# Kernel optimization log

Hardware: AMD Instinct MI355X
Metric: run time of the kernel (lower is better)

The kernel has to match this reference:

```python
import jax, jax.numpy as jnp
import numpy as np

N_ELEC, N_NUC, D, F, E = 1024, 256, 64, 64, 131072
HH, HG = 128, 128
# labels: en (elec->nuc), ne (nuc->elec), same (elec->elec), anti (elec->elec)
SRC_N = [N_ELEC, N_NUC, N_ELEC, N_ELEC]
TGT_N = [N_NUC, N_ELEC, N_ELEC, N_ELEC]


def setup_inputs() -> dict:
    key = jax.random.key(0)
    ks = jax.random.split(key, 16)
    s_elec = jax.random.normal(ks[0], (N_ELEC, D), jnp.float32)
    v_elec = jax.random.normal(ks[1], (N_ELEC, D, 3), jnp.float32)
    s_nuc = jax.random.normal(ks[2], (N_NUC, D), jnp.float32)
    v_nuc = jax.random.normal(ks[3], (N_NUC, D, 3), jnp.float32)
    senders = jnp.stack([jax.random.randint(jax.random.fold_in(ks[4], i), (E,), 0, SRC_N[i]) for i in range(4)]).astype(jnp.int32)
    receivers = jnp.stack([jax.random.randint(jax.random.fold_in(ks[5], i), (E,), 0, TGT_N[i]) for i in range(4)]).astype(jnp.int32)
    dist = jax.random.uniform(ks[6], (4, E, F), jnp.float32)
    dirs = jax.random.normal(ks[7], (4, E, 3), jnp.float32)
    dirs = dirs / jnp.linalg.norm(dirs, axis=-1, keepdims=True)  # unit directions
    def w_init(k, shape):
        return jax.random.normal(k, shape, jnp.float32) / jnp.sqrt(jnp.float32(shape[-2]))
    return {
        's_elec': s_elec, 'v_elec': v_elec, 's_nuc': s_nuc, 'v_nuc': v_nuc,
        'dist': dist, 'dirs': dirs,
        'W_w': w_init(ks[8], (4, F, 3 * D)),
        'W_h1': w_init(ks[9], (4, D, HH)), 'W_h2': w_init(ks[10], (4, HH, 3 * D)),
        'W_g1': w_init(ks[11], (4, 2 * D, HG)), 'W_g2': w_init(ks[12], (4, HG, 3 * D)),
        'W_V': jnp.broadcast_to(jnp.eye(D, dtype=jnp.float32), (4, D, D)),
        'W_U': jnp.broadcast_to(jnp.eye(D, dtype=jnp.float32), (4, D, D)),
        'senders': senders, 'receivers': receivers,
    }


def _painn_layer(s_elec, v_elec, s_nuc, v_nuc, dist, dirs, W_w, W_h1, W_h2, W_g1, W_g2, W_V, W_U, senders, receivers):
    src_s = [s_elec, s_nuc, s_elec, s_elec]
    src_v = [v_elec, v_nuc, v_elec, v_elec]
    ds_e = jnp.zeros_like(s_elec); dv_e = jnp.zeros_like(v_elec)
    ds_n = jnp.zeros_like(s_nuc); dv_n = jnp.zeros_like(v_nuc)
    for i in range(4):
        n_tgt = TGT_N[i]
        # edge MLPs: w (1-layer, last linear) and h (2-layer silu, last linear), bias-free
        we = dist[i] @ W_w[i]                                   # [E, 3D]
        h_all = jax.nn.silu(src_s[i] @ W_h1[i]) @ W_h2[i]        # [n_src, 3D]
        hx = h_all[senders[i]]                                   # gather per edge
        phi_s, phi_vv, phi_vs = jnp.split(we * hx, 3, axis=-1)   # each [E, D]
        z_s = jax.ops.segment_sum(phi_s, receivers[i], n_tgt)    # [n_tgt, D]
        vv = phi_vv[..., None] * src_v[i][senders[i]]            # [E, D, 3]
        vs = phi_vs[..., None] * dirs[i][:, None, :]             # [E, D, 3]
        z_v = jax.ops.segment_sum(vv + vs, receivers[i], n_tgt)  # [n_tgt, D, 3]
        Vv = jnp.einsum('ndi,df->nfi', z_v, W_V[i])
        Uv = jnp.einsum('ndi,df->nfi', z_v, W_U[i])
        g_in = jnp.concatenate([z_s, (Vv ** 2).sum(axis=-1)], axis=-1)  # [n_tgt, 2D]
        gs = jax.nn.silu(g_in @ W_g1[i]) @ W_g2[i]               # [n_tgt, 3D]
        a_ss, a_vv, a_sv = jnp.split(gs, 3, axis=-1)
        upd_v = Uv * a_vv[..., None]
        upd_s = a_sv * jnp.einsum('nfi,nfi->nf', Uv, Vv) + a_ss
        if i == 0:  # 'en' -> nuclei
            ds_n = ds_n + upd_s; dv_n = dv_n + upd_v
        else:       # 'ne','same','anti' -> electrons
            ds_e = ds_e + upd_s; dv_e = dv_e + upd_v
    s_e = s_elec + ds_e
    v_e = v_elec + dv_e
    return jnp.concatenate([s_e, v_e.reshape(N_ELEC, -1)], axis=-1)


def reference(s_elec, v_elec, s_nuc, v_nuc, dist, dirs, W_w, W_h1, W_h2, W_g1, W_g2, W_V, W_U, senders, receivers):
    return _painn_layer(s_elec, v_elec, s_nuc, v_nuc, dist, dirs, W_w, W_h1, W_h2, W_g1, W_g2, W_V, W_U, senders, receivers)
```

## Files before the change

### kernel.cpp

```cpp
#include <hip/hip_runtime.h>
#include <stdint.h>

#define E_EDGES 131072
#define NELEC 1024
#define NNUC 256
#define MAXCHUNK 256
#define NBLK 16

typedef __attribute__((ext_vector_type(8))) short short8;
typedef __attribute__((ext_vector_type(4))) short short4_t;
typedef __attribute__((ext_vector_type(4))) float float4_t;
typedef __attribute__((ext_vector_type(4))) int int4_t;

__device__ inline float silu_f(float x){ return x / (1.0f + expf(-x)); }

__device__ inline short f2bf_rne(float x){
    union { float f; uint32_t u; } a; a.f = x;
    return (short)((a.u + 0x7fffu + ((a.u >> 16) & 1u)) >> 16);
}
__device__ inline float bf2f(short h){
    union { uint32_t u; float f; } a; a.u = ((uint32_t)(uint16_t)h) << 16;
    return a.f;
}

__global__ __launch_bounds__(256) void prep_kernel(
    const float* __restrict__ s_elec, const float* __restrict__ v_elec,
    const float* __restrict__ s_nuc,
    const float* __restrict__ W_h1, const float* __restrict__ W_h2,
    const float* __restrict__ W_w,
    const int* __restrict__ receivers,
    float* __restrict__ h_out, short* __restrict__ fragH, short* __restrict__ fragL,
    int* __restrict__ bh, float* __restrict__ out)
{
    int b = blockIdx.x, tid = threadIdx.x;
    __shared__ float sls[8][64];
    __shared__ float hidls[128][8];
    __shared__ int hist[1024];

    if (b < 288){
        int t, node0;
        if (b < 32){ t = 0; node0 = b*8; }
        else if (b < 160){ t = 1; node0 = (b-32)*8; }
        else { t = 2; node0 = (b-160)*8; }
        int tp = t + 1;
        const float* src = (t == 0) ? s_nuc : s_elec;
        long hbase = (t == 0) ? 0 : (t == 1 ? (long)NNUC*192 : (long)NNUC*192 + (long)NELEC*192);
        for (int i = tid; i < 512; i += 256){ int n = i >> 6, f = i & 63; sls[n][f] = src[(node0+n)*64 + f]; }
        __syncthreads();
        {
            int j = tid & 127, nh = tid >> 7;
            const float* w1 = W_h1 + (long)tp*64*128;
            float a0=0,a1=0,a2=0,a3=0;
            #pragma unroll 8
            for (int f = 0; f < 64; f++){
                float w = w1[f*128 + j];
                a0 += sls[nh*4+0][f]*w; a1 += sls[nh*4+1][f]*w;
                a2 += sls[nh*4+2][f]*w; a3 += sls[nh*4+3][f]*w;
            }
            float4_t hv = { silu_f(a0), silu_f(a1), silu_f(a2), silu_f(a3) };
            *(float4_t*)&hidls[j][nh*4] = hv;
        }
        __syncthreads();
        if (tid < 192){
            const float* w2 = W_h2 + (long)tp*128*192;
            float acc[8] = {0,0,0,0,0,0,0,0};
            #pragma unroll 4
            for (int h = 0; h < 128; h++){
                float w = w2[h*192 + tid];
                float4_t ha = *(float4_t*)&hidls[h][0];
                float4_t hb = *(float4_t*)&hidls[h][4];
                acc[0]+=ha[0]*w; acc[1]+=ha[1]*w; acc[2]+=ha[2]*w; acc[3]+=ha[3]*w;
                acc[4]+=hb[0]*w; acc[5]+=hb[1]*w; acc[6]+=hb[2]*w; acc[7]+=hb[3]*w;
            }
            #pragma unroll
            for (int n = 0; n < 8; n++) h_out[hbase + (long)(node0+n)*192 + tid] = acc[n];
        }
    } else if (b < 291){
        int t = b - 288, tp = t + 1;
        const float* W = W_w + (long)tp*64*192;
        for (int idx = tid; idx < 12288; idx += 256){
            int j    = idx & 7;
            int lane = (idx >> 3) & 63;
            int ks   = (idx >> 9) & 1;
            int nt   = idx >> 10;
            int k = ks*32 + ((lane >> 4) & 3)*8 + j;
            int n = nt*16 + (lane & 15);
            float v = W[k*192 + n];
            short hi = f2bf_rne(v);
            short lo = f2bf_rne(v - bf2f(hi));
            fragH[t*12288 + idx] = hi;
            fragL[t*12288 + idx] = lo;
        }
    } else if (b < 547){
        int i = (b - 291)*256 + tid;
        int n = i >> 6, c4 = i & 63;
        float4_t v;
        if (c4 < 16) v = *(const float4_t*)(s_elec + n*64 + c4*4);
        else         v = *(const float4_t*)(v_elec + n*192 + (c4-16)*4);
        *(float4_t*)(out + n*256 + c4*4) = v;
    } else {
        int hb = b - 547, t = hb >> 4, blk = hb & 15;
        for (int i = tid; i < 1024; i += 256) hist[i] = 0;
        __syncthreads();
        long base = (long)(t+1)*E_EDGES + blk*8192;
        #pragma unroll 4
        for (int it = 0; it < 32; it++){
            int r = receivers[base + it*256 + tid];
            atomicAdd(&hist[r], 1);
        }
        __syncthreads();
        for (int bin = tid; bin < 1024; bin += 256)
            bh[(t*1024 + bin)*NBLK + blk] = hist[bin];
    }
}

__global__ __launch_bounds__(1024) void scan_kernel(int* __restrict__ bh,
                                                    int* __restrict__ offs,
                                                    int* __restrict__ counts){
    __shared__ int buf[1024];
    int tid = threadIdx.x;
    int base = tid*48;
    int vals[48];
    const int4_t* p = (const int4_t*)(bh + base);
    int s = 0;
    #pragma unroll
    for (int j = 0; j < 12; j++){
        int4_t x = p[j];
        vals[j*4+0]=x[0]; vals[j*4+1]=x[1]; vals[j*4+2]=x[2]; vals[j*4+3]=x[3];
        s += x[0]+x[1]+x[2]+x[3];
    }
    buf[tid] = s;
    __syncthreads();
    int x = s;
    for (int off = 1; off < 1024; off <<= 1){
        int y = (tid >= off) ? buf[tid - off] : 0;
        __syncthreads();
        x += y; buf[tid] = x;
        __syncthreads();
    }
    int run = x - s;
    #pragma unroll
    for (int k = 0; k < 3; k++){
        int tb = tid*3 + k;
        offs[tb] = run;
        int c = 0;
        #pragma unroll
        for (int j = 0; j < 16; j++){
            int v = vals[k*16 + j];
            bh[base + k*16 + j] = run;
            run += v; c += v;
        }
        counts[tb] = c;
    }
}

__global__ __launch_bounds__(256) void scatter_kernel(const int* __restrict__ receivers,
                                                      const int* __restrict__ senders,
                                                      const int* __restrict__ bh,
                                                      int* __restrict__ sorted){
    int hb = blockIdx.x, t = hb >> 4, blk = hb & 15;
    int tid = threadIdx.x;
    __shared__ int cur[1024];
    for (int bin = tid; bin < 1024; bin += 256) cur[bin] = bh[(t*1024 + bin)*NBLK + blk];
    __syncthreads();
    long base = (long)(t+1)*E_EDGES + blk*8192;
    #pragma unroll 2
    for (int it = 0; it < 32; it++){
        int e = blk*8192 + it*256 + tid;
        int r = receivers[base + it*256 + tid];
        int snd = senders[base + it*256 + tid];
        int pos = atomicAdd(&cur[r], 1);
        sorted[pos] = e | (snd << 17);
    }
}

__global__ __launch_bounds__(256) void main_kernel(
    const float* __restrict__ dist, const float* __restrict__ dirs,
    const float* __restrict__ v_elec, const float* __restrict__ v_nuc,
    const float* __restrict__ W_V, const float* __restrict__ W_U,
    const float* __restrict__ W_g1, const float* __restrict__ W_g2,
    const float* __restrict__ h_tab, const short* __restrict__ fragH, const short* __restrict__ fragL,
    const int* __restrict__ counts, const int* __restrict__ offs, const int* __restrict__ sorted,
    float* __restrict__ out)
{
    int b = blockIdx.x;
    int t = b >> 10;
    int node = b & 1023;
    int tp = t + 1;
    const float* v_src = (t == 0) ? v_nuc : v_elec;
    long hbase = (t == 0) ? 0 : (t == 1 ? (long)NNUC*192 : (long)NNUC*192 + (long)NELEC*192);
    const float* hsrc = h_tab + hbase;

    int tid = threadIdx.x;
    int w = tid >> 6, l = tid & 63;
    int q = l >> 4, c16 = l & 15;
    int d = w*16 + c16;

    __shared__ short AH[2][2][64][8];
    __shared__ short AL[2][2][64][8];
    __shared__ float dls[2][16][3];
    __shared__ int eid[MAXCHUNK];
    __shared__ int sid[MAXCHUNK];
    __shared__ float zs[64];
    __shared__ float zv[64][3];
    __shared__ float VvL[192], UvL[192];
    __shared__ float gin[128], hidl[128], aL[192], vdotL[64];

    short8 bhf[3][2], blf[3][2];
    #pragma unroll
    for (int ni = 0; ni < 3; ni++){
        int nt = w + ni*4;
        #pragma unroll
        for (int ks = 0; ks < 2; ks++){
            long base = (long)t*12288 + ((nt*2 + ks)*64 + l)*8;
            bhf[ni][ks] = *(const short8*)(fragH + base);
            blf[ni][ks] = *(const short8*)(fragL + base);
        }
    }

    float acc_s = 0.f, acc_v0 = 0.f, acc_v1 = 0.f, acc_v2 = 0.f;

    int deg   = counts[t*1024 + node];
    int start = offs[t*1024 + node];

    int m = tid >> 4, seg = tid & 15;
    int ks_w = seg >> 3, quad_w = (seg >> 1) & 3, j0_w = (seg & 1)*4;
    int lane2 = m | (quad_w << 4);
    int mm = tid / 3, ii = tid - mm*3;

    for (int cbase = 0; cbase < deg; cbase += MAXCHUNK){
        int chunk = deg - cbase; if (chunk > MAXCHUNK) chunk = MAXCHUNK;
        __syncthreads();
        {
            int v = 0;
            if (tid < chunk) v = sorted[(long)start + cbase + tid];
            eid[tid] = v & 131071;
            sid[tid] = v >> 17;
        }
        __syncthreads();

        int ngroups = (chunk + 15) >> 4;
        float4_t dv = {0.f,0.f,0.f,0.f};
        if (m < chunk) dv = *(const float4_t*)(dist + ((long)tp*E_EDGES + eid[m])*64 + seg*4);
        float dirv = 0.f;
        if (tid < 48 && mm < chunk) dirv = dirs[((long)tp*E_EDGES + eid[mm])*3 + ii];

        for (int g = 0; g < ngroups; g++){
            int buf = g & 1;
            {
                short4_t h4, l4;
                #pragma unroll
                for (int jj = 0; jj < 4; jj++){
                    short hi = f2bf_rne(dv[jj]);
                    h4[jj] = hi;
                    l4[jj] = f2bf_rne(dv[jj] - bf2f(hi));
                }
                *(short4_t*)&AH[buf][ks_w][lane2][j0_w] = h4;
                *(short4_t*)&AL[buf][ks_w][lane2][j0_w] = l4;
                if (tid < 48) dls[buf][mm][ii] = dirv;
            }
            float4_t dvn = {0.f,0.f,0.f,0.f};
            float dirn = 0.f;
            if (g + 1 < ngroups){
                int li = (g+1)*16 + m;
                if (li < chunk) dvn = *(const float4_t*)(dist + ((long)tp*E_EDGES + eid[li])*64 + seg*4);
                int li2 = (g+1)*16 + mm;
                if (tid < 48 && li2 < chunk) dirn = dirs[((long)tp*E_EDGES + eid[li2])*3 + ii];
            }
            __syncthreads();

            int sA[4];
            float hg[4][3], vg[4][3];
            #pragma unroll
            for (int reg = 0; reg < 4; reg++){
                int mr = q*4 + reg;
                int s = sid[g*16 + mr];
                sA[reg] = mr;
                const float* hp = hsrc + (long)s*192;
                hg[reg][0] = hp[d]; hg[reg][1] = hp[64 + d]; hg[reg][2] = hp[128 + d];
                const float* vp = v_src + (long)s*192 + d*3;
                vg[reg][0] = vp[0]; vg[reg][1] = vp[1]; vg[reg][2] = vp[2];
            }

            short8 ah0 = *(short8*)&AH[buf][0][l][0];
            short8 ah1 = *(short8*)&AH[buf][1][l][0];
            short8 al0 = *(short8*)&AL[buf][0][l][0];
            short8 al1 = *(short8*)&AL[buf][1][l][0];
            float4_t C[3];
            #pragma unroll
            for (int ni = 0; ni < 3; ni++){
                float4_t acc = {0.f,0.f,0.f,0.f};
                acc = __builtin_amdgcn_mfma_f32_16x16x32_bf16(ah0, bhf[ni][0], acc, 0, 0, 0);
                acc = __builtin_amdgcn_mfma_f32_16x16x32_bf16(ah1, bhf[ni][1], acc, 0, 0, 0);
                acc = __builtin_amdgcn_mfma_f32_16x16x32_bf16(ah0, blf[ni][0], acc, 0, 0, 0);
                acc = __builtin_amdgcn_mfma_f32_16x16x32_bf16(ah1, blf[ni][1], acc, 0, 0, 0);
                acc = __builtin_amdgcn_mfma_f32_16x16x32_bf16(al0, bhf[ni][0], acc, 0, 0, 0);
                acc = __builtin_amdgcn_mfma_f32_16x16x32_bf16(al1, bhf[ni][1], acc, 0, 0, 0);
                C[ni] = acc;
            }
            #pragma unroll
            for (int reg = 0; reg < 4; reg++){
                int mr = sA[reg];
                acc_s += C[0][reg] * hg[reg][0];
                float pvv = C[1][reg] * hg[reg][1];
                acc_v0 += pvv * vg[reg][0];
                acc_v1 += pvv * vg[reg][1];
                acc_v2 += pvv * vg[reg][2];
                float pvs = C[2][reg] * hg[reg][2];
                acc_v0 += pvs * dls[buf][mr][0];
                acc_v1 += pvs * dls[buf][mr][1];
                acc_v2 += pvs * dls[buf][mr][2];
            }
            dv = dvn; dirv = dirn;
        }
    }

    acc_s  += __shfl_xor(acc_s, 16);  acc_s  += __shfl_xor(acc_s, 32);
    acc_v0 += __shfl_xor(acc_v0, 16); acc_v0 += __shfl_xor(acc_v0, 32);
    acc_v1 += __shfl_xor(acc_v1, 16); acc_v1 += __shfl_xor(acc_v1, 32);
    acc_v2 += __shfl_xor(acc_v2, 16); acc_v2 += __shfl_xor(acc_v2, 32);
    __syncthreads();
    if (l < 16){
        zs[d] = acc_s;
        zv[d][0] = acc_v0; zv[d][1] = acc_v1; zv[d][2] = acc_v2;
    }
    __syncthreads();

    if (tid < 192){
        int i = tid >> 6, f = tid & 63;
        const float* wv = W_V + (long)tp*64*64;
        const float* wu = W_U + (long)tp*64*64;
        float av = 0.f, au = 0.f;
        #pragma unroll 8
        for (int dd = 0; dd < 64; dd++){
            float z = zv[dd][i];
            av += z * wv[dd*64 + f];
            au += z * wu[dd*64 + f];
        }
        VvL[f*3 + i] = av;
        UvL[f*3 + i] = au;
    }
    __syncthreads();
    if (tid < 64){
        int f = tid;
        float v0 = VvL[f*3], v1 = VvL[f*3+1], v2 = VvL[f*3+2];
        float u0 = UvL[f*3], u1 = UvL[f*3+1], u2 = UvL[f*3+2];
        gin[f] = zs[f];
        gin[64 + f] = v0*v0 + v1*v1 + v2*v2;
        vdotL[f] = u0*v0 + u1*v1 + u2*v2;
    }
    __syncthreads();
    if (tid < 128){
        const float* w1 = W_g1 + (long)tp*128*128;
        float acc = 0.f;
        #pragma unroll 8
        for (int c = 0; c < 128; c++) acc += gin[c] * w1[c*128 + tid];
        hidl[tid] = silu_f(acc);
    }
    __syncthreads();
    if (tid < 192){
        const float* w2 = W_g2 + (long)tp*128*192;
        float acc = 0.f;
        #pragma unroll 8
        for (int h = 0; h < 128; h++) acc += hidl[h] * w2[h*192 + tid];
        aL[tid] = acc;
    }
    __syncthreads();
    if (tid < 64){
        int f = tid;
        float upd = aL[128 + f] * vdotL[f] + aL[f];
        atomicAdd(&out[node*256 + f], upd);
    }
    if (tid < 192){
        int i = tid >> 6, f = tid & 63;
        float updv = UvL[f*3 + i] * aL[64 + f];
        atomicAdd(&out[node*256 + 64 + f*3 + i], updv);
    }
}

extern "C" void kernel_launch(void* const* d_in, const int* in_sizes, int n_in,
                              void* d_out, int out_size, void* d_ws, size_t ws_size,
                              hipStream_t stream){
    const float* s_elec  = (const float*)d_in[0];
    const float* v_elec  = (const float*)d_in[1];
    const float* s_nuc   = (const float*)d_in[2];
    const float* v_nuc   = (const float*)d_in[3];
    const float* dist    = (const float*)d_in[4];
    const float* dirs    = (const float*)d_in[5];
    const float* W_w     = (const float*)d_in[6];
    const float* W_h1    = (const float*)d_in[7];
    const float* W_h2    = (const float*)d_in[8];
    const float* W_g1    = (const float*)d_in[9];
    const float* W_g2    = (const float*)d_in[10];
    const float* W_V     = (const float*)d_in[11];
    const float* W_U     = (const float*)d_in[12];
    const int* senders   = (const int*)d_in[13];
    const int* receivers = (const int*)d_in[14];
    float* out = (float*)d_out;
    char* ws = (char*)d_ws;

    float* h_tab  = (float*)(ws + 0);
    short* fragH  = (short*)(ws + 1769472);
    short* fragL  = (short*)(ws + 1843200);
    int*   bh     = (int*)  (ws + 1916928);
    int*   offs   = (int*)  (ws + 2113536);
    int*   counts = (int*)  (ws + 2125824);
    int*   sorted = (int*)  (ws + 2138112);
    if (ws_size < 3710976) return;

    prep_kernel<<<dim3(595), dim3(256), 0, stream>>>(
        s_elec, v_elec, s_nuc, W_h1, W_h2, W_w, receivers,
        h_tab, fragH, fragL, bh, out);
    scan_kernel<<<dim3(1), dim3(1024), 0, stream>>>(bh, offs, counts);
    scatter_kernel<<<dim3(48), dim3(256), 0, stream>>>(receivers, senders, bh, sorted);
    main_kernel<<<dim3(3072), dim3(256), 0, stream>>>(
        dist, dirs, v_elec, v_nuc, W_V, W_U, W_g1, W_g2,
        h_tab, fragH, fragL, counts, offs, sorted, out);
}
```

Before: 371.9 us.

## Load edge fragments per wave directly into registers, dropping LDS staging and barriers

```diff
diff --git a/kernel.cpp b/kernel.cpp
--- a/kernel.cpp
+++ b/kernel.cpp
@@ -4,11 +4,9 @@
 #define E_EDGES 131072
 #define NELEC 1024
 #define NNUC 256
-#define MAXCHUNK 256
 #define NBLK 16
 
 typedef __attribute__((ext_vector_type(8))) short short8;
-typedef __attribute__((ext_vector_type(4))) short short4_t;
 typedef __attribute__((ext_vector_type(4))) float float4_t;
 typedef __attribute__((ext_vector_type(4))) int int4_t;
 
@@ -21,6 +19,21 @@
 __device__ inline float bf2f(short h){
     union { uint32_t u; float f; } a; a.u = ((uint32_t)(uint16_t)h) << 16;
     return a.f;
+}
+
+__device__ inline void cvt_split8(float4_t x0, float4_t x1, short8& hi, short8& lo){
+    union U8 { short8 s; uint32_t u[4]; } H, L;
+    float f[8] = {x0[0],x0[1],x0[2],x0[3],x1[0],x1[1],x1[2],x1[3]};
+    #pragma unroll
+    for (int k = 0; k < 4; k++){
+        union { float f; uint32_t u; } a, b, am, bm, la, lb;
+        a.f = f[2*k]; b.f = f[2*k+1];
+        am.u = a.u & 0xFFFF0000u; bm.u = b.u & 0xFFFF0000u;
+        H.u[k] = __builtin_amdgcn_perm(b.u, a.u, 0x07060302u);
+        la.f = a.f - am.f; lb.f = b.f - bm.f;
+        L.u[k] = __builtin_amdgcn_perm(lb.u, la.u, 0x07060302u);
+    }
+    hi = H.s; lo = L.s;
 }
 
 __global__ __launch_bounds__(256) void prep_kernel(
@@ -174,7 +187,7 @@
     }
 }
 
-__global__ __launch_bounds__(256) void main_kernel(
+__global__ __launch_bounds__(256, 3) void main_kernel(
     const float* __restrict__ dist, const float* __restrict__ dirs,
     const float* __restrict__ v_elec, const float* __restrict__ v_nuc,
     const float* __restrict__ W_V, const float* __restrict__ W_U,
@@ -184,23 +197,18 @@
     float* __restrict__ out)
 {
     int b = blockIdx.x;
-    int t = b >> 10;
-    int node = b & 1023;
-    int tp = t + 1;
+    int t = b >> 10, node = b & 1023, tp = t + 1;
     const float* v_src = (t == 0) ? v_nuc : v_elec;
     long hbase = (t == 0) ? 0 : (t == 1 ? (long)NNUC*192 : (long)NNUC*192 + (long)NELEC*192);
     const float* hsrc = h_tab + hbase;
+    const float* dbase = dist + (long)tp*E_EDGES*64;
+    const float* dirbase = dirs + (long)tp*E_EDGES*3;
 
     int tid = threadIdx.x;
     int w = tid >> 6, l = tid & 63;
     int q = l >> 4, c16 = l & 15;
     int d = w*16 + c16;
 
-    __shared__ short AH[2][2][64][8];
-    __shared__ short AL[2][2][64][8];
-    __shared__ float dls[2][16][3];
-    __shared__ int eid[MAXCHUNK];
-    __shared__ int sid[MAXCHUNK];
     __shared__ float zs[64];
     __shared__ float zv[64][3];
     __shared__ float VvL[192], UvL[192];
@@ -222,104 +230,93 @@
 
     int deg   = counts[t*1024 + node];
     int start = offs[t*1024 + node];
-
-    int m = tid >> 4, seg = tid & 15;
-    int ks_w = seg >> 3, quad_w = (seg >> 1) & 3, j0_w = (seg & 1)*4;
-    int lane2 = m | (quad_w << 4);
-    int mm = tid / 3, ii = tid - mm*3;
-
-    for (int cbase = 0; cbase < deg; cbase += MAXCHUNK){
-        int chunk = deg - cbase; if (chunk > MAXCHUNK) chunk = MAXCHUNK;
-        __syncthreads();
-        {
-            int v = 0;
-            if (tid < chunk) v = sorted[(long)start + cbase + tid];
-            eid[tid] = v & 131071;
-            sid[tid] = v >> 17;
-        }
-        __syncthreads();
-
-        int ngroups = (chunk + 15) >> 4;
-        float4_t dv = {0.f,0.f,0.f,0.f};
-        if (m < chunk) dv = *(const float4_t*)(dist + ((long)tp*E_EDGES + eid[m])*64 + seg*4);
-        float dirv = 0.f;
-        if (tid < 48 && mm < chunk) dirv = dirs[((long)tp*E_EDGES + eid[mm])*3 + ii];
-
-        for (int g = 0; g < ngroups; g++){
-            int buf = g & 1;
-            {
-                short4_t h4, l4;
-                #pragma unroll
-                for (int jj = 0; jj < 4; jj++){
-                    short hi = f2bf_rne(dv[jj]);
-                    h4[jj] = hi;
-                    l4[jj] = f2bf_rne(dv[jj] - bf2f(hi));
-                }
-                *(short4_t*)&AH[buf][ks_w][lane2][j0_w] = h4;
-                *(short4_t*)&AL[buf][ks_w][lane2][j0_w] = l4;
-                if (tid < 48) dls[buf][mm][ii] = dirv;
-            }
-            float4_t dvn = {0.f,0.f,0.f,0.f};
-            float dirn = 0.f;
-            if (g + 1 < ngroups){
-                int li = (g+1)*16 + m;
-                if (li < chunk) dvn = *(const float4_t*)(dist + ((long)tp*E_EDGES + eid[li])*64 + seg*4);
-                int li2 = (g+1)*16 + mm;
-                if (tid < 48 && li2 < chunk) dirn = dirs[((long)tp*E_EDGES + eid[li2])*3 + ii];
-            }
-            __syncthreads();
-
-            int sA[4];
-            float hg[4][3], vg[4][3];
-            #pragma unroll
-            for (int reg = 0; reg < 4; reg++){
-                int mr = q*4 + reg;
-                int s = sid[g*16 + mr];
-                sA[reg] = mr;
-                const float* hp = hsrc + (long)s*192;
-                hg[reg][0] = hp[d]; hg[reg][1] = hp[64 + d]; hg[reg][2] = hp[128 + d];
-                const float* vp = v_src + (long)s*192 + d*3;
-                vg[reg][0] = vp[0]; vg[reg][1] = vp[1]; vg[reg][2] = vp[2];
-            }
-
-            short8 ah0 = *(short8*)&AH[buf][0][l][0];
-            short8 ah1 = *(short8*)&AH[buf][1][l][0];
-            short8 al0 = *(short8*)&AL[buf][0][l][0];
-            short8 al1 = *(short8*)&AL[buf][1][l][0];
-            float4_t C[3];
-            #pragma unroll
-            for (int ni = 0; ni < 3; ni++){
-                float4_t acc = {0.f,0.f,0.f,0.f};
-                acc = __builtin_amdgcn_mfma_f32_16x16x32_bf16(ah0, bhf[ni][0], acc, 0, 0, 0);
-                acc = __builtin_amdgcn_mfma_f32_16x16x32_bf16(ah1, bhf[ni][1], acc, 0, 0, 0);
-                acc = __builtin_amdgcn_mfma_f32_16x16x32_bf16(ah0, blf[ni][0], acc, 0, 0, 0);
-                acc = __builtin_amdgcn_mfma_f32_16x16x32_bf16(ah1, blf[ni][1], acc, 0, 0, 0);
-                acc = __builtin_amdgcn_mfma_f32_16x16x32_bf16(al0, bhf[ni][0], acc, 0, 0, 0);
-                acc = __builtin_amdgcn_mfma_f32_16x16x32_bf16(al1, bhf[ni][1], acc, 0, 0, 0);
-                C[ni] = acc;
-            }
-            #pragma unroll
-            for (int reg = 0; reg < 4; reg++){
-                int mr = sA[reg];
-                acc_s += C[0][reg] * hg[reg][0];
-                float pvv = C[1][reg] * hg[reg][1];
-                acc_v0 += pvv * vg[reg][0];
-                acc_v1 += pvv * vg[reg][1];
-                acc_v2 += pvv * vg[reg][2];
-                float pvs = C[2][reg] * hg[reg][2];
-                acc_v0 += pvs * dls[buf][mr][0];
-                acc_v1 += pvs * dls[buf][mr][1];
-                acc_v2 += pvs * dls[buf][mr][2];
-            }
-            dv = dvn; dirv = dirn;
-        }
+    int ngroups = (deg + 15) >> 4;
+
+    const float4_t z4 = {0.f,0.f,0.f,0.f};
+    int seC = 0;
+    float4_t A0 = z4, A1 = z4, A2 = z4, A3 = z4;
+
+    if (ngroups > 0){
+        int rel = c16;
+        int idx = start + (rel < deg ? rel : deg - 1);
+        seC = sorted[idx];
+        const float* rp = dbase + (long)(seC & 131071)*64 + q*8;
+        A0 = *(const float4_t*)(rp);
+        A1 = *(const float4_t*)(rp + 4);
+        A2 = *(const float4_t*)(rp + 32);
+        A3 = *(const float4_t*)(rp + 36);
+        if (rel >= deg){ A0 = z4; A1 = z4; A2 = z4; A3 = z4; }
+    }
+
+    for (int g = 0; g < ngroups; g++){
+        int seN = 0;
+        float4_t N0 = z4, N1 = z4, N2 = z4, N3 = z4;
+        if (g + 1 < ngroups){
+            int rel = (g+1)*16 + c16;
+            int idx = start + (rel < deg ? rel : deg - 1);
+            seN = sorted[idx];
+            const float* rp = dbase + (long)(seN & 131071)*64 + q*8;
+            N0 = *(const float4_t*)(rp);
+            N1 = *(const float4_t*)(rp + 4);
+            N2 = *(const float4_t*)(rp + 32);
+            N3 = *(const float4_t*)(rp + 36);
+            if (rel >= deg){ N0 = z4; N1 = z4; N2 = z4; N3 = z4; }
+        }
+
+        const float* dp = dirbase + (long)(seC & 131071)*3;
+        float dr0 = dp[0], dr1 = dp[1], dr2 = dp[2];
+
+        float hg[4][3], vg[4][3];
+        #pragma unroll
+        for (int reg = 0; reg < 4; reg++){
+            int sse = __shfl(seC, q*4 + reg, 64);
+            int s = ((unsigned)sse) >> 17;
+            const float* hp = hsrc + (long)s*192 + d;
+            hg[reg][0] = hp[0]; hg[reg][1] = hp[64]; hg[reg][2] = hp[128];
+            const float* vp = v_src + (long)s*192 + d*3;
+            vg[reg][0] = vp[0]; vg[reg][1] = vp[1]; vg[reg][2] = vp[2];
+        }
+
+        short8 ah0, al0, ah1, al1;
+        cvt_split8(A0, A1, ah0, al0);
+        cvt_split8(A2, A3, ah1, al1);
+        float4_t C[3];
+        #pragma unroll
+        for (int ni = 0; ni < 3; ni++){
+            float4_t acc = z4;
+            acc = __builtin_amdgcn_mfma_f32_16x16x32_bf16(ah0, bhf[ni][0], acc, 0, 0, 0);
+            acc = __builtin_amdgcn_mfma_f32_16x16x32_bf16(ah1, bhf[ni][1], acc, 0, 0, 0);
+            acc = __builtin_amdgcn_mfma_f32_16x16x32_bf16(ah0, blf[ni][0], acc, 0, 0, 0);
+            acc = __builtin_amdgcn_mfma_f32_16x16x32_bf16(ah1, blf[ni][1], acc, 0, 0, 0);
+            acc = __builtin_amdgcn_mfma_f32_16x16x32_bf16(al0, bhf[ni][0], acc, 0, 0, 0);
+            acc = __builtin_amdgcn_mfma_f32_16x16x32_bf16(al1, bhf[ni][1], acc, 0, 0, 0);
+            C[ni] = acc;
+        }
+
+        #pragma unroll
+        for (int reg = 0; reg < 4; reg++){
+            int src = q*4 + reg;
+            float e0 = __shfl(dr0, src, 64);
+            float e1 = __shfl(dr1, src, 64);
+            float e2 = __shfl(dr2, src, 64);
+            acc_s += C[0][reg] * hg[reg][0];
+            float pvv = C[1][reg] * hg[reg][1];
+            acc_v0 += pvv * vg[reg][0];
+            acc_v1 += pvv * vg[reg][1];
+            acc_v2 += pvv * vg[reg][2];
+            float pvs = C[2][reg] * hg[reg][2];
+            acc_v0 += pvs * e0;
+            acc_v1 += pvs * e1;
+            acc_v2 += pvs * e2;
+        }
+
+        seC = seN; A0 = N0; A1 = N1; A2 = N2; A3 = N3;
     }
 
     acc_s  += __shfl_xor(acc_s, 16);  acc_s  += __shfl_xor(acc_s, 32);
     acc_v0 += __shfl_xor(acc_v0, 16); acc_v0 += __shfl_xor(acc_v0, 32);
     acc_v1 += __shfl_xor(acc_v1, 16); acc_v1 += __shfl_xor(acc_v1, 32);
     acc_v2 += __shfl_xor(acc_v2, 16); acc_v2 += __shfl_xor(acc_v2, 32);
-    __syncthreads();
     if (l < 16){
         zs[d] = acc_s;
         zv[d][0] = acc_v0; zv[d][1] = acc_v1; zv[d][2] = acc_v2;
```

New measurement: 405.0 us. 8.9% more time.

## Precompute packed bf16 sender tables with h*v products and prefetch gathers

Applied to the files above, without the earlier changes.

```diff
diff --git a/kernel.cpp b/kernel.cpp
--- a/kernel.cpp
+++ b/kernel.cpp
@@ -7,10 +7,12 @@
 #define MAXCHUNK 256
 #define NBLK 16
 
+typedef unsigned short ushort_t;
 typedef __attribute__((ext_vector_type(8))) short short8;
 typedef __attribute__((ext_vector_type(4))) short short4_t;
 typedef __attribute__((ext_vector_type(4))) float float4_t;
 typedef __attribute__((ext_vector_type(4))) int int4_t;
+typedef __attribute__((ext_vector_type(2))) unsigned int uint2_t;
 
 __device__ inline float silu_f(float x){ return x / (1.0f + expf(-x)); }
 
@@ -22,14 +24,18 @@
     union { uint32_t u; float f; } a; a.u = ((uint32_t)(uint16_t)h) << 16;
     return a.f;
 }
+__device__ inline ushort_t bfu(float x){ return (ushort_t)f2bf_rne(x); }
+__device__ inline float asf_lo(uint32_t u){ union { uint32_t u; float f; } a; a.u = u << 16; return a.f; }
+__device__ inline float asf_hi(uint32_t u){ union { uint32_t u; float f; } a; a.u = u & 0xFFFF0000u; return a.f; }
 
 __global__ __launch_bounds__(256) void prep_kernel(
     const float* __restrict__ s_elec, const float* __restrict__ v_elec,
-    const float* __restrict__ s_nuc,
+    const float* __restrict__ s_nuc,  const float* __restrict__ v_nuc,
     const float* __restrict__ W_h1, const float* __restrict__ W_h2,
     const float* __restrict__ W_w,
     const int* __restrict__ receivers,
-    float* __restrict__ h_out, short* __restrict__ fragH, short* __restrict__ fragL,
+    ushort_t* __restrict__ tabA, ushort_t* __restrict__ tabB,
+    short* __restrict__ fragH, short* __restrict__ fragL,
     int* __restrict__ bh, float* __restrict__ out)
 {
     int b = blockIdx.x, tid = threadIdx.x;
@@ -44,7 +50,9 @@
         else { t = 2; node0 = (b-160)*8; }
         int tp = t + 1;
         const float* src = (t == 0) ? s_nuc : s_elec;
-        long hbase = (t == 0) ? 0 : (t == 1 ? (long)NNUC*192 : (long)NNUC*192 + (long)NELEC*192);
+        const float* vsrc = (t == 0) ? v_nuc : v_elec;
+        long baseA = (t == 0) ? 0 : (t == 1 ? 32768 : 163840);
+        long baseB = (t == 0) ? 0 : (t == 1 ? 65536 : 327680);
         for (int i = tid; i < 512; i += 256){ int n = i >> 6, f = i & 63; sls[n][f] = src[(node0+n)*64 + f]; }
         __syncthreads();
         {
@@ -72,8 +80,25 @@
                 acc[0]+=ha[0]*w; acc[1]+=ha[1]*w; acc[2]+=ha[2]*w; acc[3]+=ha[3]*w;
                 acc[4]+=hb[0]*w; acc[5]+=hb[1]*w; acc[6]+=hb[2]*w; acc[7]+=hb[3]*w;
             }
-            #pragma unroll
-            for (int n = 0; n < 8; n++) h_out[hbase + (long)(node0+n)*192 + tid] = acc[n];
+            int p = tid >> 6, d2 = tid & 63;
+            if (p == 0){
+                #pragma unroll
+                for (int n = 0; n < 8; n++)
+                    tabA[baseA + (long)((node0+n)*64 + d2)*2 + 0] = bfu(acc[n]);
+            } else if (p == 2){
+                #pragma unroll
+                for (int n = 0; n < 8; n++)
+                    tabA[baseA + (long)((node0+n)*64 + d2)*2 + 1] = bfu(acc[n]);
+            } else {
+                #pragma unroll
+                for (int n = 0; n < 8; n++){
+                    const float* vp = vsrc + (long)(node0+n)*192 + d2*3;
+                    long o = baseB + (long)((node0+n)*64 + d2)*4;
+                    tabB[o+0] = bfu(acc[n]*vp[0]);
+                    tabB[o+1] = bfu(acc[n]*vp[1]);
+                    tabB[o+2] = bfu(acc[n]*vp[2]);
+                }
+            }
         }
     } else if (b < 291){
         int t = b - 288, tp = t + 1;
@@ -176,20 +201,19 @@
 
 __global__ __launch_bounds__(256) void main_kernel(
     const float* __restrict__ dist, const float* __restrict__ dirs,
-    const float* __restrict__ v_elec, const float* __restrict__ v_nuc,
     const float* __restrict__ W_V, const float* __restrict__ W_U,
     const float* __restrict__ W_g1, const float* __restrict__ W_g2,
-    const float* __restrict__ h_tab, const short* __restrict__ fragH, const short* __restrict__ fragL,
+    const ushort_t* __restrict__ tabA, const ushort_t* __restrict__ tabB,
+    const short* __restrict__ fragH, const short* __restrict__ fragL,
     const int* __restrict__ counts, const int* __restrict__ offs, const int* __restrict__ sorted,
     float* __restrict__ out)
 {
     int b = blockIdx.x;
-    int t = b >> 10;
-    int node = b & 1023;
-    int tp = t + 1;
-    const float* v_src = (t == 0) ? v_nuc : v_elec;
-    long hbase = (t == 0) ? 0 : (t == 1 ? (long)NNUC*192 : (long)NNUC*192 + (long)NELEC*192);
-    const float* hsrc = h_tab + hbase;
+    int t = b >> 10, node = b & 1023, tp = t + 1;
+    const ushort_t* ta = tabA + ((t == 0) ? 0 : (t == 1 ? 32768 : 163840));
+    const ushort_t* tb = tabB + ((t == 0) ? 0 : (t == 1 ? 65536 : 327680));
+    const float* dbase = dist + (long)tp*E_EDGES*64;
+    const float* dirbase = dirs + (long)tp*E_EDGES*3;
 
     int tid = threadIdx.x;
     int w = tid >> 6, l = tid & 63;
@@ -228,6 +252,8 @@
     int lane2 = m | (quad_w << 4);
     int mm = tid / 3, ii = tid - mm*3;
 
+    const float4_t z4 = {0.f,0.f,0.f,0.f};
+
     for (int cbase = 0; cbase < deg; cbase += MAXCHUNK){
         int chunk = deg - cbase; if (chunk > MAXCHUNK) chunk = MAXCHUNK;
         __syncthreads();
@@ -235,15 +261,22 @@
             int v = 0;
             if (tid < chunk) v = sorted[(long)start + cbase + tid];
             eid[tid] = v & 131071;
-            sid[tid] = v >> 17;
+            sid[tid] = ((unsigned)v) >> 17;
         }
         __syncthreads();
 
         int ngroups = (chunk + 15) >> 4;
-        float4_t dv = {0.f,0.f,0.f,0.f};
-        if (m < chunk) dv = *(const float4_t*)(dist + ((long)tp*E_EDGES + eid[m])*64 + seg*4);
+        float4_t dv = z4;
+        if (m < chunk) dv = *(const float4_t*)(dbase + (long)eid[m]*64 + seg*4);
         float dirv = 0.f;
-        if (tid < 48 && mm < chunk) dirv = dirs[((long)tp*E_EDGES + eid[mm])*3 + ii];
+        if (tid < 48 && mm < chunk) dirv = dirbase[(long)eid[mm]*3 + ii];
+        uint32_t gA[4]; uint2_t gB[4];
+        #pragma unroll
+        for (int r = 0; r < 4; r++){
+            int s = sid[q*4 + r];
+            gA[r] = *(const uint32_t*)(ta + (long)(s*64 + d)*2);
+            gB[r] = *(const uint2_t*)(tb + (long)(s*64 + d)*4);
+        }
 
         for (int g = 0; g < ngroups; g++){
             int buf = g & 1;
@@ -259,28 +292,21 @@
                 *(short4_t*)&AL[buf][ks_w][lane2][j0_w] = l4;
                 if (tid < 48) dls[buf][mm][ii] = dirv;
             }
-            float4_t dvn = {0.f,0.f,0.f,0.f};
-            float dirn = 0.f;
+            float4_t dvn = z4; float dirn = 0.f;
+            uint32_t gAn[4] = {0,0,0,0}; uint2_t gBn[4] = {{0,0},{0,0},{0,0},{0,0}};
             if (g + 1 < ngroups){
                 int li = (g+1)*16 + m;
-                if (li < chunk) dvn = *(const float4_t*)(dist + ((long)tp*E_EDGES + eid[li])*64 + seg*4);
+                if (li < chunk) dvn = *(const float4_t*)(dbase + (long)eid[li]*64 + seg*4);
                 int li2 = (g+1)*16 + mm;
-                if (tid < 48 && li2 < chunk) dirn = dirs[((long)tp*E_EDGES + eid[li2])*3 + ii];
+                if (tid < 48 && li2 < chunk) dirn = dirbase[(long)eid[li2]*3 + ii];
+                #pragma unroll
+                for (int r = 0; r < 4; r++){
+                    int s = sid[(g+1)*16 + q*4 + r];
+                    gAn[r] = *(const uint32_t*)(ta + (long)(s*64 + d)*2);
+                    gBn[r] = *(const uint2_t*)(tb + (long)(s*64 + d)*4);
+                }
             }
             __syncthreads();
-
-            int sA[4];
-            float hg[4][3], vg[4][3];
-            #pragma unroll
-            for (int reg = 0; reg < 4; reg++){
-                int mr = q*4 + reg;
-                int s = sid[g*16 + mr];
-                sA[reg] = mr;
-                const float* hp = hsrc + (long)s*192;
-                hg[reg][0] = hp[d]; hg[reg][1] = hp[64 + d]; hg[reg][2] = hp[128 + d];
-                const float* vp = v_src + (long)s*192 + d*3;
-                vg[reg][0] = vp[0]; vg[reg][1] = vp[1]; vg[reg][2] = vp[2];
-            }
 
             short8 ah0 = *(short8*)&AH[buf][0][l][0];
             short8 ah1 = *(short8*)&AH[buf][1][l][0];
@@ -289,7 +315,7 @@
             float4_t C[3];
             #pragma unroll
             for (int ni = 0; ni < 3; ni++){
-                float4_t acc = {0.f,0.f,0.f,0.f};
+                float4_t acc = z4;
                 acc = __builtin_amdgcn_mfma_f32_16x16x32_bf16(ah0, bhf[ni][0], acc, 0, 0, 0);
                 acc = __builtin_amdgcn_mfma_f32_16x16x32_bf16(ah1, bhf[ni][1], acc, 0, 0, 0);
                 acc = __builtin_amdgcn_mfma_f32_16x16x32_bf16(ah0, blf[ni][0], acc, 0, 0, 0);
@@ -298,20 +324,24 @@
                 acc = __builtin_amdgcn_mfma_f32_16x16x32_bf16(al1, bhf[ni][1], acc, 0, 0, 0);
                 C[ni] = acc;
             }
+
             #pragma unroll
-            for (int reg = 0; reg < 4; reg++){
-                int mr = sA[reg];
-                acc_s += C[0][reg] * hg[reg][0];
-                float pvv = C[1][reg] * hg[reg][1];
-                acc_v0 += pvv * vg[reg][0];
-                acc_v1 += pvv * vg[reg][1];
-                acc_v2 += pvv * vg[reg][2];
-                float pvs = C[2][reg] * hg[reg][2];
-                acc_v0 += pvs * dls[buf][mr][0];
-                acc_v1 += pvs * dls[buf][mr][1];
-                acc_v2 += pvs * dls[buf][mr][2];
+            for (int r = 0; r < 4; r++){
+                int mr = q*4 + r;
+                float hs  = asf_lo(gA[r]);
+                float hvs = asf_hi(gA[r]);
+                float hv0 = asf_lo(gB[r][0]);
+                float hv1 = asf_hi(gB[r][0]);
+                float hv2 = asf_lo(gB[r][1]);
+                acc_s += C[0][r] * hs;
+                float pvs = C[2][r] * hvs;
+                acc_v0 += C[1][r]*hv0 + pvs * dls[buf][mr][0];
+                acc_v1 += C[1][r]*hv1 + pvs * dls[buf][mr][1];
+                acc_v2 += C[1][r]*hv2 + pvs * dls[buf][mr][2];
             }
             dv = dvn; dirv = dirn;
+            #pragma unroll
+            for (int r = 0; r < 4; r++){ gA[r] = gAn[r]; gB[r] = gBn[r]; }
         }
     }
 
@@ -399,7 +429,8 @@
     float* out = (float*)d_out;
     char* ws = (char*)d_ws;
 
-    float* h_tab  = (float*)(ws + 0);
+    ushort_t* tabA  = (ushort_t*)(ws + 0);
+    ushort_t* tabB  = (ushort_t*)(ws + 589824);
     short* fragH  = (short*)(ws + 1769472);
     short* fragL  = (short*)(ws + 1843200);
     int*   bh     = (int*)  (ws + 1916928);
@@ -409,11 +440,11 @@
     if (ws_size < 3710976) return;
 
     prep_kernel<<<dim3(595), dim3(256), 0, stream>>>(
-        s_elec, v_elec, s_nuc, W_h1, W_h2, W_w, receivers,
-        h_tab, fragH, fragL, bh, out);
+        s_elec, v_elec, s_nuc, v_nuc, W_h1, W_h2, W_w, receivers,
+        tabA, tabB, fragH, fragL, bh, out);
     scan_kernel<<<dim3(1), dim3(1024), 0, stream>>>(bh, offs, counts);
     scatter_kernel<<<dim3(48), dim3(256), 0, stream>>>(receivers, senders, bh, sorted);
     main_kernel<<<dim3(3072), dim3(256), 0, stream>>>(
-        dist, dirs, v_elec, v_nuc, W_V, W_U, W_g1, W_g2,
-        h_tab, fragH, fragL, counts, offs, sorted, out);
-}
+        dist, dirs, W_V, W_U, W_g1, W_g2,
+        tabA, tabB, fragH, fragL, counts, offs, sorted, out);
+}
```

Result: faster. 363.3 us (-2.3%).
